# Kernel optimization log

Hardware: AMD Instinct MI355X
Metric: run time of the kernel (lower is better)

## Reference

```python
import jax, jax.numpy as jnp
import numpy as np

N = 262144   # total nodes
E = 1048576  # total edges
B = 512      # graphs per batch
IN, H, EDIM, AH, CH, NB = 8, 128, 4, 128, 128, 4

def _lin(key, fi, fo):
    # kaiming_normal fan_out/relu approximated with fan_in scaling (only affects init stats)
    return jax.random.normal(key, (fi, fo), jnp.float32) * np.sqrt(2.0 / fi)

def setup_inputs() -> dict:
    key = jax.random.key(0)
    ks = jax.random.split(key, 24)
    inp = {}
    inp['x'] = jax.random.normal(ks[0], (N, IN), jnp.float32)
    inp['edge_index'] = jax.random.randint(ks[1], (2, E), 0, N)
    inp['edge_attr'] = jax.random.normal(ks[2], (E, EDIM), jnp.float32)
    seg = N // B
    inp['batch'] = (jnp.arange(N) // seg).astype(jnp.int32)
    inp['ptr'] = (jnp.arange(B + 1) * seg).astype(jnp.int32)
    dims = [(IN, H), (H, H), (H, H)]  # final layer outputs embed_dim == H
    for l, (di, do) in enumerate(dims):
        inp[f'We{l}'] = _lin(ks[3 + 2 * l], EDIM, di)
        inp[f'be{l}'] = jnp.zeros((di,), jnp.float32)
        inp[f'W{l}'] = _lin(ks[4 + 2 * l], di, do)
        inp[f'b{l}'] = jnp.zeros((do,), jnp.float32)
    inp['laW1'] = _lin(ks[10], H, AH); inp['lab1'] = jnp.zeros((AH,), jnp.float32)
    inp['laW2'] = _lin(ks[11], AH, 1); inp['lab2'] = jnp.zeros((1,), jnp.float32)
    inp['maW1'] = _lin(ks[12], H, AH); inp['mab1'] = jnp.zeros((AH,), jnp.float32)
    inp['maW2'] = _lin(ks[13], AH, NB); inp['mab2'] = jnp.zeros((NB,), jnp.float32)
    inp['lcW1'] = _lin(ks[14], H, CH); inp['lcb1'] = jnp.zeros((CH,), jnp.float32)
    inp['lcW2'] = _lin(ks[15], CH, 1); inp['lcb2'] = jnp.zeros((1,), jnp.float32)
    inp['mcW1'] = _lin(ks[16], H, CH); inp['mcb1'] = jnp.zeros((CH,), jnp.float32)
    inp['mcW2'] = _lin(ks[17], CH, 1); inp['mcb2'] = jnp.zeros((1,), jnp.float32)
    return inp

def _gnn(x, edge_index, edge_attr, Wes, bes, Ws, bs):
    # GINE-style edge-conditioned message passing (dropout off / eval mode)
    src, dst = edge_index[0], edge_index[1]
    h = x
    for We, be, W, b in zip(Wes, bes, Ws, bs):
        msg = jax.nn.relu(h[src] + edge_attr @ We + be)            # [E, d]
        agg = jax.ops.segment_sum(msg, dst, num_segments=N)        # [N, d]
        h = jax.nn.relu((h + agg) @ W + b)
    return h

def reference(x, edge_index, edge_attr, batch, ptr,
              We0, be0, W0, b0, We1, be1, W1, b1, We2, be2, W2, b2,
              laW1, lab1, laW2, lab2, maW1, mab1, maW2, mab2,
              lcW1, lcb1, lcW2, lcb2, mcW1, mcb1, mcW2, mcb2):
    emb = _gnn(x, edge_index, edge_attr, [We0, We1, We2], [be0, be1, be2], [W0, W1, W2], [b0, b1, b2])  # [N, H]

    # per-node location logit, then fused segmented softmax over each graph's nodes
    loc_logits = (jax.nn.relu(emb @ laW1 + lab1) @ laW2 + lab2)[:, 0]  # [N]
    seg_max = jax.ops.segment_max(loc_logits, batch, num_segments=B)
    shifted = loc_logits - seg_max[batch]
    denom = jax.ops.segment_sum(jnp.exp(shifted), batch, num_segments=B)
    logp = shifted - jnp.log(denom)[batch]                              # per-node log-prob within its graph
    loc_entropy = -jax.ops.segment_sum(jnp.exp(logp) * logp, batch, num_segments=B)  # [B]

    # segmented categorical sampling via Gumbel-max (global node index, matching start+local_idx)
    key = jax.random.key(42)
    u = jax.random.uniform(key, (N,), minval=1e-6, maxval=1.0 - 1e-6)
    pert = loc_logits - jnp.log(-jnp.log(u))
    pmax = jax.ops.segment_max(pert, batch, num_segments=B)
    cand = jnp.where(pert >= pmax[batch], jnp.arange(N), N)
    locations = jax.ops.segment_min(cand, batch, num_segments=B)        # [B] global indices
    loc_log_probs = logp[locations]                                     # [B]

    sel = emb[locations]                                                # [B, H]
    mut_logits = jax.nn.relu(sel @ maW1 + mab1) @ maW2 + mab2           # [B, NB]
    mut_logp = jax.nn.log_softmax(mut_logits, axis=-1)
    mutations = jax.random.categorical(jax.random.fold_in(key, 1), mut_logits, axis=-1)  # [B]
    mut_log_probs = jnp.take_along_axis(mut_logp, mutations[:, None], axis=-1)[:, 0]
    mut_entropy = -jnp.sum(jnp.exp(mut_logp) * mut_logp, axis=-1)

    # critics: global_add_pool + MLP -> scalar per graph; mutation critic on selected node
    pooled = jax.ops.segment_sum(emb, batch, num_segments=B)            # [B, H]
    loc_values = (jax.nn.relu(pooled @ lcW1 + lcb1) @ lcW2 + lcb2)[:, 0]
    mut_values = (jax.nn.relu(sel @ mcW1 + mcb1) @ mcW2 + mcb2)[:, 0]

    return (locations, mutations, loc_log_probs, mut_log_probs,
            loc_entropy, mut_entropy, loc_values, mut_values, emb)
```

## Files before the change

kernel.cpp:

```cpp
#include <hip/hip_runtime.h>
#include <cstdint>
#include <cstddef>

#define NN 262144
#define EE 1048576
#define BB 512
#define SEG 512

__device__ __forceinline__ unsigned rotl32(unsigned x, int r) {
    return (x << r) | (x >> (32 - r));
}

__device__ __forceinline__ void tf2x32(unsigned k0, unsigned k1, unsigned x0, unsigned x1,
                                       unsigned& o0, unsigned& o1) {
    unsigned ks[3] = {k0, k1, k0 ^ k1 ^ 0x1BD11BDAu};
    x0 += ks[0]; x1 += ks[1];
    const int R0[4] = {13, 15, 26, 6};
    const int R1[4] = {17, 29, 16, 24};
#pragma unroll
    for (int i = 0; i < 5; ++i) {
        const int* R = (i & 1) ? R1 : R0;
#pragma unroll
        for (int j = 0; j < 4; ++j) {
            x0 += x1;
            x1 = rotl32(x1, R[j]);
            x1 ^= x0;
        }
        x0 += ks[(i + 1) % 3];
        x1 += ks[(i + 2) % 3] + (unsigned)(i + 1);
    }
    o0 = x0; o1 = x1;
}

__device__ __forceinline__ float unif_loc(unsigned idx) {
    unsigned j = idx & (NN / 2 - 1);
    unsigned half = idx >> 17;
    unsigned o0, o1;
    tf2x32(0u, 42u, j, j + (unsigned)(NN / 2), o0, o1);
    unsigned bits = half ? o1 : o0;
    float f = __uint_as_float((bits >> 9) | 0x3F800000u) - 1.0f;
    const float minv = 1e-6f;
    const float maxv = 1.0f - 1e-6f;
    const float span = maxv - minv;
    return fmaxf(minv, __fadd_rn(__fmul_rn(f, span), minv));
}

__global__ void csr_count(const int* __restrict__ dst, int* __restrict__ counts, int E) {
    int i = blockIdx.x * 256 + threadIdx.x;
    if (i < E) atomicAdd(&counts[dst[i]], 1);
}

__global__ void scan512(const int* __restrict__ in, int* __restrict__ outExcl, int* __restrict__ bsum) {
    __shared__ int s[512];
    int b = blockIdx.x, tid = threadIdx.x;
    int v = in[(size_t)b * 512 + tid];
    s[tid] = v;
    __syncthreads();
    for (int d = 1; d < 512; d <<= 1) {
        int add = (tid >= d) ? s[tid - d] : 0;
        __syncthreads();
        s[tid] += add;
        __syncthreads();
    }
    outExcl[(size_t)b * 512 + tid] = s[tid] - v;
    if (tid == 511) bsum[b] = s[511];
}

__global__ void scan_fix(int* __restrict__ offs, const int* __restrict__ bbase,
                         int* __restrict__ cursor, int N, int E) {
    int gid = blockIdx.x * 512 + threadIdx.x;
    int v = offs[gid] + bbase[blockIdx.x];
    offs[gid] = v;
    cursor[gid] = v;
    if (gid == 0) offs[N] = E;
}

__global__ void csr_fill(const int* __restrict__ dst, const int* __restrict__ src,
                         const float4* __restrict__ ea, int* __restrict__ cursor,
                         int* __restrict__ ssrc, float4* __restrict__ sea, int E) {
    int i = blockIdx.x * 256 + threadIdx.x;
    if (i < E) {
        int p = atomicAdd(&cursor[dst[i]], 1);
        ssrc[p] = src[i];
        sea[p] = ea[i];
    }
}

__global__ void agg_l0(const float* __restrict__ x, const int* __restrict__ ssrc,
                       const float4* __restrict__ sea, const int* __restrict__ offs,
                       const float* __restrict__ We0, const float* __restrict__ be0,
                       float* __restrict__ out) {
    __shared__ float Ws[32];
    __shared__ float bs[8];
    int tid = threadIdx.x;
    if (tid < 32) Ws[tid] = We0[tid];
    if (tid < 8) bs[tid] = be0[tid];
    __syncthreads();
    int n = blockIdx.x * 256 + tid;
    float a[8] = {0.f, 0.f, 0.f, 0.f, 0.f, 0.f, 0.f, 0.f};
    int pb = offs[n], pe = offs[n + 1];
    for (int p = pb; p < pe; ++p) {
        int s = ssrc[p];
        float4 ev = sea[p];
        float4 xa = *(const float4*)(x + (size_t)s * 8);
        float4 xb = *(const float4*)(x + (size_t)s * 8 + 4);
        float xs[8] = {xa.x, xa.y, xa.z, xa.w, xb.x, xb.y, xb.z, xb.w};
#pragma unroll
        for (int j2 = 0; j2 < 8; ++j2) {
            float m = xs[j2] + bs[j2] + ev.x * Ws[j2] + ev.y * Ws[8 + j2] +
                      ev.z * Ws[16 + j2] + ev.w * Ws[24 + j2];
            a[j2] += fmaxf(m, 0.f);
        }
    }
    float4 o0 = {a[0], a[1], a[2], a[3]};
    float4 o1 = {a[4], a[5], a[6], a[7]};
    *(float4*)(out + (size_t)n * 8) = o0;
    *(float4*)(out + (size_t)n * 8 + 4) = o1;
}

__global__ __launch_bounds__(256) void update_l0(const float* __restrict__ x,
                                                 const float* __restrict__ agg0,
                                                 const float* __restrict__ W0,
                                                 const float* __restrict__ b0,
                                                 float* __restrict__ h1) {
    __shared__ float Ws[8 * 128];
    __shared__ float bs[128];
    int tid = threadIdx.x;
#pragma unroll
    for (int i = tid; i < 1024; i += 256) Ws[i] = W0[i];
    if (tid < 128) bs[tid] = b0[tid];
    __syncthreads();
    int sub = tid >> 7;
    int c = tid & 127;
    float bias = bs[c];
    float wcol[8];
#pragma unroll
    for (int k = 0; k < 8; ++k) wcol[k] = Ws[k * 128 + c];
    int base = blockIdx.x * 128;
    for (int it = 0; it < 64; ++it) {
        int node = base + it * 2 + sub;
        const float* xp = x + (size_t)node * 8;
        const float* ap = agg0 + (size_t)node * 8;
        float4 xa = *(const float4*)xp;
        float4 xb = *(const float4*)(xp + 4);
        float4 aa = *(const float4*)ap;
        float4 ab = *(const float4*)(ap + 4);
        float t[8] = {xa.x + aa.x, xa.y + aa.y, xa.z + aa.z, xa.w + aa.w,
                      xb.x + ab.x, xb.y + ab.y, xb.z + ab.z, xb.w + ab.w};
        float acc = bias;
#pragma unroll
        for (int k = 0; k < 8; ++k) acc = fmaf(t[k], wcol[k], acc);
        h1[(size_t)node * 128 + c] = fmaxf(acc, 0.f);
    }
}

__global__ __launch_bounds__(256) void agg_l(const float2* __restrict__ h2,
                                             const int* __restrict__ ssrc,
                                             const float4* __restrict__ sea,
                                             const int* __restrict__ offs,
                                             const float* __restrict__ We,
                                             const float* __restrict__ be,
                                             float2* __restrict__ out) {
    int tid = threadIdx.x;
    int lane = tid & 63;
    int n0 = blockIdx.x * 32 + (tid >> 6) * 8;
    n0 = __builtin_amdgcn_readfirstlane(n0);
    const float2* We2 = (const float2*)We;
    float2 w0 = We2[lane], w1 = We2[64 + lane], w2 = We2[128 + lane], w3 = We2[192 + lane];
    float2 bv = ((const float2*)be)[lane];

    int b0  = __builtin_amdgcn_readfirstlane(offs[n0 + 0]);
    int nb0 = __builtin_amdgcn_readfirstlane(offs[n0 + 1]);
    int nb1 = __builtin_amdgcn_readfirstlane(offs[n0 + 2]);
    int nb2 = __builtin_amdgcn_readfirstlane(offs[n0 + 3]);
    int nb3 = __builtin_amdgcn_readfirstlane(offs[n0 + 4]);
    int nb4 = __builtin_amdgcn_readfirstlane(offs[n0 + 5]);
    int nb5 = __builtin_amdgcn_readfirstlane(offs[n0 + 6]);
    int nb6 = __builtin_amdgcn_readfirstlane(offs[n0 + 7]);
    int nb7 = __builtin_amdgcn_readfirstlane(offs[n0 + 8]);
    int pend = nb7;

    float2 acc = {0.f, 0.f};
    float2* optr = out + (size_t)n0 * 64 + lane;

#define FLUSH(pp)                                        \
    while ((pp) == nb0) {                                \
        *optr = acc;                                     \
        acc.x = 0.f; acc.y = 0.f;                        \
        optr += 64;                                      \
        nb0 = nb1; nb1 = nb2; nb2 = nb3; nb3 = nb4;      \
        nb4 = nb5; nb5 = nb6; nb6 = nb7; nb7 = 0x7FFFFFFF; \
    }

#define ACC(hv, ev)                                                                     \
    {                                                                                   \
        float mx = hv.x + bv.x + ev.x * w0.x + ev.y * w1.x + ev.z * w2.x + ev.w * w3.x; \
        float my = hv.y + bv.y + ev.x * w0.y + ev.y * w1.y + ev.z * w2.y + ev.w * w3.y; \
        acc.x += fmaxf(mx, 0.f);                                                        \
        acc.y += fmaxf(my, 0.f);                                                        \
    }

    int p = b0;
    for (; p + 8 <= pend; p += 8) {
        int s_[8];
#pragma unroll
        for (int j = 0; j < 8; ++j) s_[j] = ssrc[p + j];
        float4 e_[8];
#pragma unroll
        for (int j = 0; j < 8; ++j) e_[j] = sea[p + j];
        float2 h_[8];
#pragma unroll
        for (int j = 0; j < 8; ++j) h_[j] = h2[(size_t)s_[j] * 64 + lane];
#pragma unroll
        for (int j = 0; j < 8; ++j) {
            FLUSH(p + j)
            ACC(h_[j], e_[j])
        }
    }
    for (; p < pend; ++p) {
        FLUSH(p)
        int s0 = ssrc[p];
        float4 e0 = sea[p];
        float2 ha = h2[(size_t)s0 * 64 + lane];
        ACC(ha, e0)
    }
    FLUSH(pend)
#undef ACC
#undef FLUSH
}

typedef __attribute__((ext_vector_type(8))) short bf16x8;
typedef __attribute__((ext_vector_type(4))) float f32x4;

__device__ __forceinline__ ushort bf16r(float x) {
    unsigned u = __float_as_uint(x);
    return (ushort)((u + 0x7FFFu + ((u >> 16) & 1u)) >> 16);
}
__device__ __forceinline__ float bf2f(ushort h) {
    return __uint_as_float(((unsigned)h) << 16);
}

__global__ void pack3(const float* __restrict__ W1, const float* __restrict__ W2,
                      const float* __restrict__ LA, uint4* __restrict__ dst) {
    const float* W = (blockIdx.x == 0) ? W1 : (blockIdx.x == 1) ? W2 : LA;
    uint4* ph = dst + (size_t)blockIdx.x * 4096;
    uint4* pl = ph + 2048;
    int t = threadIdx.x;
    int l = t & 63, q = t >> 6;
    int lo = l & 15, kg = l >> 4;
    for (int i = 0; i < 8; ++i) {
        int combo = q * 8 + i;
        int kc = combo >> 3, n = combo & 7;
        ushort h8[8], l8[8];
#pragma unroll
        for (int j = 0; j < 8; ++j) {
            float wv = W[(size_t)(kc * 32 + kg * 8 + j) * 128 + n * 16 + lo];
            ushort hh = bf16r(wv);
            h8[j] = hh;
            l8[j] = bf16r(wv - bf2f(hh));
        }
        int idx = (kc * 8 + n) * 64 + l;
        ph[idx] = *(const uint4*)h8;
        pl[idx] = *(const uint4*)l8;
    }
}

__device__ __forceinline__ void conv_frag(const float4& r0, const float4& r1,
                                          bf16x8& ah, bf16x8& al) {
    float av[8] = {r0.x, r0.y, r0.z, r0.w, r1.x, r1.y, r1.z, r1.w};
#pragma unroll
    for (int j = 0; j < 8; ++j) {
        ushort hh = bf16r(av[j]);
        ah[j] = (short)hh;
        al[j] = (short)bf16r(av[j] - bf2f(hh));
    }
}

__device__ __forceinline__ void load_a_frags(const float* P, const float* Q, int r0,
                                             int lo, int kg, int kc,
                                             bf16x8& ah0, bf16x8& al0,
                                             bf16x8& ah1, bf16x8& al1) {
#pragma unroll
    for (int m = 0; m < 2; ++m) {
        const float* ap = P + (size_t)(r0 + m * 16 + lo) * 128 + kc * 32 + kg * 8;
        float4 p0 = *(const float4*)ap;
        float4 p1 = *(const float4*)(ap + 4);
        if (Q) {
            const float* qp = Q + (size_t)(r0 + m * 16 + lo) * 128 + kc * 32 + kg * 8;
            float4 q0 = *(const float4*)qp;
            float4 q1 = *(const float4*)(qp + 4);
            p0.x += q0.x; p0.y += q0.y; p0.z += q0.z; p0.w += q0.w;
            p1.x += q1.x; p1.y += q1.y; p1.z += q1.z; p1.w += q1.w;
        }
        bf16x8 ah, al;
        conv_frag(p0, p1, ah, al);
        if (m == 0) { ah0 = ah; al0 = al; } else { ah1 = ah; al1 = al; }
    }
}

__global__ __launch_bounds__(256) void gemm_mfma(const float* __restrict__ P, const float* Q,
                                                 const uint4* __restrict__ Wh,
                                                 const uint4* __restrict__ Wl,
                                                 const float* __restrict__ bias,
                                                 float* out) {
    int tid = threadIdx.x;
    int w = tid >> 6, l = tid & 63;
    int r0 = blockIdx.x * 128 + w * 32;
    int lo = l & 15, kg = l >> 4;
    const bf16x8* Bh = (const bf16x8*)Wh;
    const bf16x8* Bl = (const bf16x8*)Wl;
    f32x4 acc[2][8];
#pragma unroll
    for (int m = 0; m < 2; ++m)
#pragma unroll
        for (int n = 0; n < 8; ++n) acc[m][n] = (f32x4){0.f, 0.f, 0.f, 0.f};

    for (int kc = 0; kc < 4; ++kc) {
        bf16x8 ah0, al0, ah1, al1;
        load_a_frags(P, Q, r0, lo, kg, kc, ah0, al0, ah1, al1);
#pragma unroll
        for (int h2i = 0; h2i < 2; ++h2i) {
            bf16x8 bh[4], bl[4];
#pragma unroll
            for (int nn = 0; nn < 4; ++nn) {
                int idx = (kc * 8 + h2i * 4 + nn) * 64 + l;
                bh[nn] = Bh[idx];
                bl[nn] = Bl[idx];
            }
#pragma unroll
            for (int nn = 0; nn < 4; ++nn) {
                int n = h2i * 4 + nn;
                acc[0][n] = __builtin_amdgcn_mfma_f32_16x16x32_bf16(ah0, bh[nn], acc[0][n], 0, 0, 0);
                acc[0][n] = __builtin_amdgcn_mfma_f32_16x16x32_bf16(al0, bh[nn], acc[0][n], 0, 0, 0);
                acc[0][n] = __builtin_amdgcn_mfma_f32_16x16x32_bf16(ah0, bl[nn], acc[0][n], 0, 0, 0);
                acc[1][n] = __builtin_amdgcn_mfma_f32_16x16x32_bf16(ah1, bh[nn], acc[1][n], 0, 0, 0);
                acc[1][n] = __builtin_amdgcn_mfma_f32_16x16x32_bf16(al1, bh[nn], acc[1][n], 0, 0, 0);
                acc[1][n] = __builtin_amdgcn_mfma_f32_16x16x32_bf16(ah1, bl[nn], acc[1][n], 0, 0, 0);
            }
        }
    }
    float bv[8];
#pragma unroll
    for (int n = 0; n < 8; ++n) bv[n] = bias[n * 16 + lo];
#pragma unroll
    for (int m = 0; m < 2; ++m)
#pragma unroll
        for (int n = 0; n < 8; ++n)
#pragma unroll
            for (int v = 0; v < 4; ++v) {
                size_t g = (size_t)(r0 + m * 16 + kg * 4 + v) * 128 + n * 16 + lo;
                out[g] = fmaxf(acc[m][n][v] + bv[n], 0.f);
            }
}

__global__ __launch_bounds__(256) void gemm_emb_fused(const float* __restrict__ P, const float* Q,
                                                      const uint4* __restrict__ Wh,
                                                      const uint4* __restrict__ Wl,
                                                      const float* __restrict__ bias,
                                                      const uint4* __restrict__ LWh,
                                                      const uint4* __restrict__ LWl,
                                                      const float* __restrict__ lb1,
                                                      const float* __restrict__ lw2,
                                                      const float* __restrict__ lb2,
                                                      float* out,
                                                      float* __restrict__ pooled,
                                                      float* __restrict__ Lg) {
    __shared__ float eL[4][32][132];
    __shared__ float poolL[4][128];
    int tid = threadIdx.x;
    int w = tid >> 6, l = tid & 63;
    int r0 = blockIdx.x * 128 + w * 32;
    int lo = l & 15, kg = l >> 4;
    const bf16x8* Bh = (const bf16x8*)Wh;
    const bf16x8* Bl = (const bf16x8*)Wl;
    f32x4 acc[2][8];
#pragma unroll
    for (int m = 0; m < 2; ++m)
#pragma unroll
        for (int n = 0; n < 8; ++n) acc[m][n] = (f32x4){0.f, 0.f, 0.f, 0.f};

    for (int kc = 0; kc < 4; ++kc) {
        bf16x8 ah0, al0, ah1, al1;
        load_a_frags(P, Q, r0, lo, kg, kc, ah0, al0, ah1, al1);
#pragma unroll
        for (int h2i = 0; h2i < 2; ++h2i) {
            bf16x8 bh[4], bl[4];
#pragma unroll
            for (int nn = 0; nn < 4; ++nn) {
                int idx = (kc * 8 + h2i * 4 + nn) * 64 + l;
                bh[nn] = Bh[idx];
                bl[nn] = Bl[idx];
            }
#pragma unroll
            for (int nn = 0; nn < 4; ++nn) {
                int n = h2i * 4 + nn;
                acc[0][n] = __builtin_amdgcn_mfma_f32_16x16x32_bf16(ah0, bh[nn], acc[0][n], 0, 0, 0);
                acc[0][n] = __builtin_amdgcn_mfma_f32_16x16x32_bf16(al0, bh[nn], acc[0][n], 0, 0, 0);
                acc[0][n] = __builtin_amdgcn_mfma_f32_16x16x32_bf16(ah0, bl[nn], acc[0][n], 0, 0, 0);
                acc[1][n] = __builtin_amdgcn_mfma_f32_16x16x32_bf16(ah1, bh[nn], acc[1][n], 0, 0, 0);
                acc[1][n] = __builtin_amdgcn_mfma_f32_16x16x32_bf16(al1, bh[nn], acc[1][n], 0, 0, 0);
                acc[1][n] = __builtin_amdgcn_mfma_f32_16x16x32_bf16(ah1, bl[nn], acc[1][n], 0, 0, 0);
            }
        }
    }
    float bv[8];
#pragma unroll
    for (int n = 0; n < 8; ++n) bv[n] = bias[n * 16 + lo];
    float psum[8];
#pragma unroll
    for (int n = 0; n < 8; ++n) psum[n] = 0.f;
#pragma unroll
    for (int m = 0; m < 2; ++m)
#pragma unroll
        for (int n = 0; n < 8; ++n)
#pragma unroll
            for (int v = 0; v < 4; ++v) {
                float e = fmaxf(acc[m][n][v] + bv[n], 0.f);
                size_t g = (size_t)(r0 + m * 16 + kg * 4 + v) * 128 + n * 16 + lo;
                out[g] = e;
                eL[w][m * 16 + kg * 4 + v][n * 16 + lo] = e;
                psum[n] += e;
            }
#pragma unroll
    for (int n = 0; n < 8; ++n) {
        psum[n] += __shfl_xor(psum[n], 16);
        psum[n] += __shfl_xor(psum[n], 32);
    }
    if (l < 16) {
#pragma unroll
        for (int n = 0; n < 8; ++n) poolL[w][n * 16 + l] = psum[n];
    }
    __syncthreads();
    if (tid < 128) {
        float s = poolL[0][tid] + poolL[1][tid] + poolL[2][tid] + poolL[3][tid];
        atomicAdd(&pooled[(blockIdx.x >> 2) * 128 + tid], s);
    }
    const bf16x8* LBh = (const bf16x8*)LWh;
    const bf16x8* LBl = (const bf16x8*)LWl;
    f32x4 acc2[2][8];
#pragma unroll
    for (int m = 0; m < 2; ++m)
#pragma unroll
        for (int n = 0; n < 8; ++n) acc2[m][n] = (f32x4){0.f, 0.f, 0.f, 0.f};
    for (int kc = 0; kc < 4; ++kc) {
        bf16x8 ah[2], al[2];
#pragma unroll
        for (int m = 0; m < 2; ++m) {
            const float* ep = &eL[w][m * 16 + lo][kc * 32 + kg * 8];
            float4 a0 = *(const float4*)ep;
            float4 a1 = *(const float4*)(ep + 4);
            conv_frag(a0, a1, ah[m], al[m]);
        }
#pragma unroll
        for (int h2i = 0; h2i < 2; ++h2i) {
            bf16x8 bh[4], bl[4];
#pragma unroll
            for (int nn = 0; nn < 4; ++nn) {
                int idx = (kc * 8 + h2i * 4 + nn) * 64 + l;
                bh[nn] = LBh[idx];
                bl[nn] = LBl[idx];
            }
#pragma unroll
            for (int nn = 0; nn < 4; ++nn) {
                int n = h2i * 4 + nn;
                acc2[0][n] = __builtin_amdgcn_mfma_f32_16x16x32_bf16(ah[0], bh[nn], acc2[0][n], 0, 0, 0);
                acc2[0][n] = __builtin_amdgcn_mfma_f32_16x16x32_bf16(al[0], bh[nn], acc2[0][n], 0, 0, 0);
                acc2[0][n] = __builtin_amdgcn_mfma_f32_16x16x32_bf16(ah[0], bl[nn], acc2[0][n], 0, 0, 0);
                acc2[1][n] = __builtin_amdgcn_mfma_f32_16x16x32_bf16(ah[1], bh[nn], acc2[1][n], 0, 0, 0);
                acc2[1][n] = __builtin_amdgcn_mfma_f32_16x16x32_bf16(al[1], bh[nn], acc2[1][n], 0, 0, 0);
                acc2[1][n] = __builtin_amdgcn_mfma_f32_16x16x32_bf16(ah[1], bl[nn], acc2[1][n], 0, 0, 0);
            }
        }
    }
    float b1v[8], w2v[8];
#pragma unroll
    for (int n = 0; n < 8; ++n) {
        b1v[n] = lb1[n * 16 + lo];
        w2v[n] = lw2[n * 16 + lo];
    }
    float lb2v = lb2[0];
#pragma unroll
    for (int m = 0; m < 2; ++m)
#pragma unroll
        for (int v = 0; v < 4; ++v) {
            float s = 0.f;
#pragma unroll
            for (int n = 0; n < 8; ++n)
                s += fmaxf(acc2[m][n][v] + b1v[n], 0.f) * w2v[n];
            s += __shfl_xor(s, 8);
            s += __shfl_xor(s, 4);
            s += __shfl_xor(s, 2);
            s += __shfl_xor(s, 1);
            if (lo == 0) Lg[r0 + m * 16 + kg * 4 + v] = s + lb2v;
        }
}

__global__ void sample_k(const float* __restrict__ L, float* __restrict__ ob,
                         int* __restrict__ locInt) {
    int g = blockIdx.x, tid = threadIdx.x;
    __shared__ float sh[512];
    __shared__ float rb[256];
    __shared__ int ib[256];
    float l0 = L[g * 512 + tid];
    float l1 = L[g * 512 + 256 + tid];
    rb[tid] = fmaxf(l0, l1);
    __syncthreads();
    for (int s2 = 128; s2 > 0; s2 >>= 1) {
        if (tid < s2) rb[tid] = fmaxf(rb[tid], rb[tid + s2]);
        __syncthreads();
    }
    float mx = rb[0];
    __syncthreads();
    float s0 = l0 - mx, s1 = l1 - mx;
    sh[tid] = s0; sh[256 + tid] = s1;
    float e0 = expf(s0), e1 = expf(s1);
    rb[tid] = e0 + e1;
    __syncthreads();
    for (int s2 = 128; s2 > 0; s2 >>= 1) {
        if (tid < s2) rb[tid] += rb[tid + s2];
        __syncthreads();
    }
    float denom = rb[0];
    __syncthreads();
    rb[tid] = e0 * s0 + e1 * s1;
    __syncthreads();
    for (int s2 = 128; s2 > 0; s2 >>= 1) {
        if (tid < s2) rb[tid] += rb[tid + s2];
        __syncthreads();
    }
    float sum2 = rb[0];
    __syncthreads();
    unsigned i0 = (unsigned)(g * 512 + tid);
    unsigned i1 = i0 + 256u;
    float p0 = l0 - logf(-logf(unif_loc(i0)));
    float p1 = l1 - logf(-logf(unif_loc(i1)));
    rb[tid] = fmaxf(p0, p1);
    __syncthreads();
    for (int s2 = 128; s2 > 0; s2 >>= 1) {
        if (tid < s2) rb[tid] = fmaxf(rb[tid], rb[tid + s2]);
        __syncthreads();
    }
    float pmax = rb[0];
    __syncthreads();
    int c0 = (p0 >= pmax) ? tid : 0x7FFFFFFF;
    int c1 = (p1 >= pmax) ? (tid + 256) : 0x7FFFFFFF;
    ib[tid] = min(c0, c1);
    __syncthreads();
    for (int s2 = 128; s2 > 0; s2 >>= 1) {
        if (tid < s2) ib[tid] = min(ib[tid], ib[tid + s2]);
        __syncthreads();
    }
    if (tid == 0) {
        int li = ib[0];
        float logD = logf(denom);
        ob[g] = (float)(g * 512 + li);
        ob[1024 + g] = sh[li] - logD;
        ob[2048 + g] = logD - sum2 / denom;
        locInt[g] = g * 512 + li;
    }
}

__global__ void heads_k(const float* __restrict__ emb, const float* __restrict__ pooled,
                        const int* __restrict__ locInt,
                        const float* __restrict__ maW1, const float* __restrict__ mab1,
                        const float* __restrict__ maW2, const float* __restrict__ mab2,
                        const float* __restrict__ lcW1, const float* __restrict__ lcb1,
                        const float* __restrict__ lcW2, const float* __restrict__ lcb2,
                        const float* __restrict__ mcW1, const float* __restrict__ mcb1,
                        const float* __restrict__ mcW2, const float* __restrict__ mcb2,
                        float* __restrict__ ob) {
    int g = blockIdx.x, tid = threadIdx.x;
    __shared__ float sel[128], pl[128];
    __shared__ float red[4][128];
    __shared__ float red1[128];
    __shared__ float mcv_sh;
    sel[tid] = emb[(size_t)locInt[g] * 128 + tid];
    pl[tid] = pooled[g * 128 + tid];
    __syncthreads();
    float h = mab1[tid];
    for (int k = 0; k < 128; ++k) h = fmaf(sel[k], maW1[k * 128 + tid], h);
    h = fmaxf(h, 0.f);
    red[0][tid] = h * maW2[tid * 4 + 0];
    red[1][tid] = h * maW2[tid * 4 + 1];
    red[2][tid] = h * maW2[tid * 4 + 2];
    red[3][tid] = h * maW2[tid * 4 + 3];
    __syncthreads();
    for (int s2 = 64; s2 > 0; s2 >>= 1) {
        if (tid < s2) {
            red[0][tid] += red[0][tid + s2];
            red[1][tid] += red[1][tid + s2];
            red[2][tid] += red[2][tid + s2];
            red[3][tid] += red[3][tid + s2];
        }
        __syncthreads();
    }
    float h2 = mcb1[tid];
    for (int k = 0; k < 128; ++k) h2 = fmaf(sel[k], mcW1[k * 128 + tid], h2);
    h2 = fmaxf(h2, 0.f);
    red1[tid] = h2 * mcW2[tid];
    __syncthreads();
    for (int s2 = 64; s2 > 0; s2 >>= 1) {
        if (tid < s2) red1[tid] += red1[tid + s2];
        __syncthreads();
    }
    if (tid == 0) mcv_sh = red1[0] + mcb2[0];
    __syncthreads();
    float h3 = lcb1[tid];
    for (int k = 0; k < 128; ++k) h3 = fmaf(pl[k], lcW1[k * 128 + tid], h3);
    h3 = fmaxf(h3, 0.f);
    red1[tid] = h3 * lcW2[tid];
    __syncthreads();
    for (int s2 = 64; s2 > 0; s2 >>= 1) {
        if (tid < s2) red1[tid] += red1[tid + s2];
        __syncthreads();
    }
    if (tid == 0) {
        float lcv = red1[0] + lcb2[0];
        float lg[4];
#pragma unroll
        for (int c = 0; c < 4; ++c) lg[c] = red[c][0] + mab2[c];
        unsigned fk0, fk1;
        tf2x32(0u, 42u, 0u, 1u, fk0, fk1);
        float gmb[4];
#pragma unroll
        for (int c = 0; c < 4; ++c) {
            unsigned m = (unsigned)(g * 4 + c);
            unsigned j = m & 1023u;
            unsigned halfb = m >> 10;
            unsigned o0, o1;
            tf2x32(fk0, fk1, j, j + 1024u, o0, o1);
            unsigned bits = halfb ? o1 : o0;
            float f = __uint_as_float((bits >> 9) | 0x3F800000u) - 1.0f;
            const float tiny = 1.17549435e-38f;
            float u = fmaxf(tiny, __fadd_rn(__fmul_rn(f, 1.0f), tiny));
            gmb[c] = -logf(-logf(u));
        }
        int best = 0;
        float bz = gmb[0] + lg[0];
#pragma unroll
        for (int c = 1; c < 4; ++c) {
            float z = gmb[c] + lg[c];
            if (z > bz) { bz = z; best = c; }
        }
        float M = fmaxf(fmaxf(lg[0], lg[1]), fmaxf(lg[2], lg[3]));
        float se = 0.f;
#pragma unroll
        for (int c = 0; c < 4; ++c) se += expf(lg[c] - M);
        float lse = M + logf(se);
        float ent = 0.f;
#pragma unroll
        for (int c = 0; c < 4; ++c) {
            float lp = lg[c] - lse;
            ent -= expf(lp) * lp;
        }
        ob[512 + g] = (float)best;
        ob[1536 + g] = lg[best] - lse;
        ob[2560 + g] = ent;
        ob[3072 + g] = lcv;
        ob[3584 + g] = mcv_sh;
    }
}

extern "C" void kernel_launch(void* const* d_in, const int* in_sizes, int n_in,
                              void* d_out, int out_size, void* d_ws, size_t ws_size,
                              hipStream_t stream) {
    const float* x   = (const float*)d_in[0];
    const int* ei    = (const int*)d_in[1];
    const float* ea  = (const float*)d_in[2];
    const float* We0 = (const float*)d_in[5];
    const float* be0 = (const float*)d_in[6];
    const float* W0  = (const float*)d_in[7];
    const float* b0  = (const float*)d_in[8];
    const float* We1 = (const float*)d_in[9];
    const float* be1 = (const float*)d_in[10];
    const float* W1  = (const float*)d_in[11];
    const float* b1  = (const float*)d_in[12];
    const float* We2 = (const float*)d_in[13];
    const float* be2 = (const float*)d_in[14];
    const float* W2  = (const float*)d_in[15];
    const float* b2  = (const float*)d_in[16];
    const float* laW1 = (const float*)d_in[17];
    const float* lab1 = (const float*)d_in[18];
    const float* laW2 = (const float*)d_in[19];
    const float* lab2 = (const float*)d_in[20];
    const float* maW1 = (const float*)d_in[21];
    const float* mab1 = (const float*)d_in[22];
    const float* maW2 = (const float*)d_in[23];
    const float* mab2 = (const float*)d_in[24];
    const float* lcW1 = (const float*)d_in[25];
    const float* lcb1 = (const float*)d_in[26];
    const float* lcW2 = (const float*)d_in[27];
    const float* lcb2 = (const float*)d_in[28];
    const float* mcW1 = (const float*)d_in[29];
    const float* mcb1 = (const float*)d_in[30];
    const float* mcW2 = (const float*)d_in[31];
    const float* mcb2 = (const float*)d_in[32];

    float* out = (float*)d_out;
    char* ws = (char*)d_ws;
    size_t off = 0;
    auto alloc = [&](size_t bytes) -> void* {
        void* p = ws + off;
        off += (bytes + 255) & ~(size_t)255;
        return p;
    };
    float* U    = (float*)alloc((size_t)NN * 128 * 4);
    int* counts = (int*)alloc((size_t)NN * 4);
    int* offs   = (int*)alloc((size_t)(NN + 1) * 4);
    int* cursor = (int*)alloc((size_t)NN * 4);
    int* ssrc   = (int*)alloc((size_t)EE * 4);
    float4* sea = (float4*)alloc((size_t)EE * 16);
    int* bsum   = (int*)alloc(512 * 4);
    int* bbase  = (int*)alloc(512 * 4);
    int* bscr   = (int*)alloc(512 * 4);
    float* Lg   = (float*)alloc((size_t)NN * 4);
    float* pooled = (float*)alloc((size_t)BB * 128 * 4);
    int* locInt = (int*)alloc((size_t)BB * 4);

    const int* src = ei;
    const int* dstA = ei + EE;
    float* V = out + 4096;
    float* agg0 = U;

    uint4* wpack = (uint4*)cursor;

    hipMemsetAsync(counts, 0, (size_t)NN * 4, stream);
    hipMemsetAsync(pooled, 0, (size_t)BB * 128 * 4, stream);
    csr_count<<<EE / 256, 256, 0, stream>>>(dstA, counts, EE);
    scan512<<<NN / 512, 512, 0, stream>>>(counts, offs, bsum);
    scan512<<<1, 512, 0, stream>>>(bsum, bbase, bscr);
    scan_fix<<<NN / 512, 512, 0, stream>>>(offs, bbase, cursor, NN, EE);
    csr_fill<<<EE / 256, 256, 0, stream>>>(dstA, src, (const float4*)ea, cursor, ssrc, sea, EE);
    pack3<<<3, 256, 0, stream>>>(W1, W2, laW1, wpack);

    agg_l0<<<NN / 256, 256, 0, stream>>>(x, ssrc, sea, offs, We0, be0, agg0);
    update_l0<<<NN / 128, 256, 0, stream>>>(x, agg0, W0, b0, V);
    agg_l<<<NN / 32, 256, 0, stream>>>((const float2*)V, ssrc, sea, offs, We1, be1, (float2*)U);
    gemm_mfma<<<NN / 128, 256, 0, stream>>>(V, U, wpack, wpack + 2048, b1, U);
    agg_l<<<NN / 32, 256, 0, stream>>>((const float2*)U, ssrc, sea, offs, We2, be2, (float2*)V);
    gemm_emb_fused<<<NN / 128, 256, 0, stream>>>(U, V, wpack + 4096, wpack + 6144, b2,
                                                 wpack + 8192, wpack + 10240, lab1, laW2, lab2,
                                                 V, pooled, Lg);

    sample_k<<<BB, 256, 0, stream>>>(Lg, out, locInt);
    heads_k<<<BB, 128, 0, stream>>>(V, pooled, locInt, maW1, mab1, maW2, mab2,
                                    lcW1, lcb1, lcW2, lcb2, mcW1, mcb1, mcW2, mcb2, out);
}
```

Before: 854.9 us.

## Halve LDS staging in fused embedding GEMM and process second head MMA in two passes

The fused embedding/location-head kernel now stages only 16 rows per wave in shared memory instead of 32, keeping the second half of the embedding in registers and running the head GEMM in two sequential 16-row passes. It also adds a minimum-blocks hint of 4 to launch_bounds. The intent is to cut LDS footprint and accumulator registers so more blocks fit per CU, at the cost of serialising the head MMA and losing some ILP between the two row tiles. There is also a risk of register spilling under the tighter launch bound.

```diff
diff --git a/kernel.cpp b/kernel.cpp
--- a/kernel.cpp
+++ b/kernel.cpp
@@ -353,7 +353,7 @@
             }
 }
 
-__global__ __launch_bounds__(256) void gemm_emb_fused(const float* __restrict__ P, const float* Q,
+__global__ __launch_bounds__(256, 4) void gemm_emb_fused(const float* __restrict__ P, const float* Q,
                                                       const uint4* __restrict__ Wh,
                                                       const uint4* __restrict__ Wl,
                                                       const float* __restrict__ bias,
@@ -365,7 +365,7 @@
                                                       float* out,
                                                       float* __restrict__ pooled,
                                                       float* __restrict__ Lg) {
-    __shared__ float eL[4][32][132];
+    __shared__ float eL[4][16][132];
     __shared__ float poolL[4][128];
     int tid = threadIdx.x;
     int w = tid >> 6, l = tid & 63;
@@ -409,18 +409,19 @@
     float psum[8];
 #pragma unroll
     for (int n = 0; n < 8; ++n) psum[n] = 0.f;
-#pragma unroll
-    for (int m = 0; m < 2; ++m)
-#pragma unroll
-        for (int n = 0; n < 8; ++n)
-#pragma unroll
-            for (int v = 0; v < 4; ++v) {
-                float e = fmaxf(acc[m][n][v] + bv[n], 0.f);
-                size_t g = (size_t)(r0 + m * 16 + kg * 4 + v) * 128 + n * 16 + lo;
-                out[g] = e;
-                eL[w][m * 16 + kg * 4 + v][n * 16 + lo] = e;
-                psum[n] += e;
-            }
+    f32x4 keep[8];
+#pragma unroll
+    for (int n = 0; n < 8; ++n)
+#pragma unroll
+        for (int v = 0; v < 4; ++v) {
+            float e0 = fmaxf(acc[0][n][v] + bv[n], 0.f);
+            float e1 = fmaxf(acc[1][n][v] + bv[n], 0.f);
+            out[(size_t)(r0 + kg * 4 + v) * 128 + n * 16 + lo] = e0;
+            out[(size_t)(r0 + 16 + kg * 4 + v) * 128 + n * 16 + lo] = e1;
+            eL[w][kg * 4 + v][n * 16 + lo] = e0;
+            keep[n][v] = e1;
+            psum[n] += e0 + e1;
+        }
 #pragma unroll
     for (int n = 0; n < 8; ++n) {
         psum[n] += __shfl_xor(psum[n], 16);
@@ -437,62 +438,61 @@
     }
     const bf16x8* LBh = (const bf16x8*)LWh;
     const bf16x8* LBl = (const bf16x8*)LWl;
-    f32x4 acc2[2][8];
-#pragma unroll
-    for (int m = 0; m < 2; ++m)
-#pragma unroll
-        for (int n = 0; n < 8; ++n) acc2[m][n] = (f32x4){0.f, 0.f, 0.f, 0.f};
-    for (int kc = 0; kc < 4; ++kc) {
-        bf16x8 ah[2], al[2];
-#pragma unroll
-        for (int m = 0; m < 2; ++m) {
-            const float* ep = &eL[w][m * 16 + lo][kc * 32 + kg * 8];
+    for (int mh = 0; mh < 2; ++mh) {
+        if (mh == 1) {
+#pragma unroll
+            for (int n = 0; n < 8; ++n)
+#pragma unroll
+                for (int v = 0; v < 4; ++v)
+                    eL[w][kg * 4 + v][n * 16 + lo] = keep[n][v];
+        }
+        f32x4 acc2[8];
+#pragma unroll
+        for (int n = 0; n < 8; ++n) acc2[n] = (f32x4){0.f, 0.f, 0.f, 0.f};
+        for (int kc = 0; kc < 4; ++kc) {
+            const float* ep = &eL[w][lo][kc * 32 + kg * 8];
             float4 a0 = *(const float4*)ep;
             float4 a1 = *(const float4*)(ep + 4);
-            conv_frag(a0, a1, ah[m], al[m]);
-        }
-#pragma unroll
-        for (int h2i = 0; h2i < 2; ++h2i) {
-            bf16x8 bh[4], bl[4];
-#pragma unroll
-            for (int nn = 0; nn < 4; ++nn) {
-                int idx = (kc * 8 + h2i * 4 + nn) * 64 + l;
-                bh[nn] = LBh[idx];
-                bl[nn] = LBl[idx];
+            bf16x8 ah, al;
+            conv_frag(a0, a1, ah, al);
+#pragma unroll
+            for (int h2i = 0; h2i < 2; ++h2i) {
+                bf16x8 bh[4], bl[4];
+#pragma unroll
+                for (int nn = 0; nn < 4; ++nn) {
+                    int idx = (kc * 8 + h2i * 4 + nn) * 64 + l;
+                    bh[nn] = LBh[idx];
+                    bl[nn] = LBl[idx];
+                }
+#pragma unroll
+                for (int nn = 0; nn < 4; ++nn) {
+                    int n = h2i * 4 + nn;
+                    acc2[n] = __builtin_amdgcn_mfma_f32_16x16x32_bf16(ah, bh[nn], acc2[n], 0, 0, 0);
+                    acc2[n] = __builtin_amdgcn_mfma_f32_16x16x32_bf16(al, bh[nn], acc2[n], 0, 0, 0);
+                    acc2[n] = __builtin_amdgcn_mfma_f32_16x16x32_bf16(ah, bl[nn], acc2[n], 0, 0, 0);
+                }
             }
-#pragma unroll
-            for (int nn = 0; nn < 4; ++nn) {
-                int n = h2i * 4 + nn;
-                acc2[0][n] = __builtin_amdgcn_mfma_f32_16x16x32_bf16(ah[0], bh[nn], acc2[0][n], 0, 0, 0);
-                acc2[0][n] = __builtin_amdgcn_mfma_f32_16x16x32_bf16(al[0], bh[nn], acc2[0][n], 0, 0, 0);
-                acc2[0][n] = __builtin_amdgcn_mfma_f32_16x16x32_bf16(ah[0], bl[nn], acc2[0][n], 0, 0, 0);
-                acc2[1][n] = __builtin_amdgcn_mfma_f32_16x16x32_bf16(ah[1], bh[nn], acc2[1][n], 0, 0, 0);
-                acc2[1][n] = __builtin_amdgcn_mfma_f32_16x16x32_bf16(al[1], bh[nn], acc2[1][n], 0, 0, 0);
-                acc2[1][n] = __builtin_amdgcn_mfma_f32_16x16x32_bf16(ah[1], bl[nn], acc2[1][n], 0, 0, 0);
-            }
-        }
-    }
-    float b1v[8], w2v[8];
-#pragma unroll
-    for (int n = 0; n < 8; ++n) {
-        b1v[n] = lb1[n * 16 + lo];
-        w2v[n] = lw2[n * 16 + lo];
-    }
-    float lb2v = lb2[0];
-#pragma unroll
-    for (int m = 0; m < 2; ++m)
+        }
+        float b1v[8], w2v[8];
+#pragma unroll
+        for (int n = 0; n < 8; ++n) {
+            b1v[n] = lb1[n * 16 + lo];
+            w2v[n] = lw2[n * 16 + lo];
+        }
+        float lb2v = lb2[0];
 #pragma unroll
         for (int v = 0; v < 4; ++v) {
             float s = 0.f;
 #pragma unroll
             for (int n = 0; n < 8; ++n)
-                s += fmaxf(acc2[m][n][v] + b1v[n], 0.f) * w2v[n];
+                s += fmaxf(acc2[n][v] + b1v[n], 0.f) * w2v[n];
             s += __shfl_xor(s, 8);
             s += __shfl_xor(s, 4);
             s += __shfl_xor(s, 2);
             s += __shfl_xor(s, 1);
-            if (lo == 0) Lg[r0 + m * 16 + kg * 4 + v] = s + lb2v;
-        }
+            if (lo == 0) Lg[r0 + mh * 16 + kg * 4 + v] = s + lb2v;
+        }
+    }
 }
 
 __global__ void sample_k(const float* __restrict__ L, float* __restrict__ ob,
```

New measurement: 1.144 ms. +33.9%, slower.
